# Kernel optimization log

Hardware: AMD Instinct MI355X
Metric: run time of the kernel (lower is better)

The kernel has to match this reference:

```python
import jax, jax.numpy as jnp
import numpy as np

LX, LY = 16, 16
N = 2 * LX * LY        # 512 lattice sites (sequence length)
NH = 128               # GRU hidden size
K = 2                  # binary occupation categories
NS = 4096              # number of Monte-Carlo samples (batch)


def setup_inputs() -> dict:
    key = jax.random.key(0)
    k0, k1, k2, k3 = jax.random.split(key, 4)
    gru_kernel = jax.random.normal(k0, (K, 3 * NH), jnp.float32) * (1.0 / np.sqrt(K))
    gru_rkernel = jax.random.normal(k1, (NH, 3 * NH), jnp.float32) * (1.0 / np.sqrt(NH))
    gru_bias = jnp.zeros((2, 3 * NH), jnp.float32)  # [input_bias; recurrent_bias] (reset_after=True)
    dense_w = jax.random.normal(k2, (NH, K), jnp.float32) * (1.0 / np.sqrt(NH))
    dense_b = jnp.zeros((K,), jnp.float32)
    u = jax.random.uniform(k3, (NS, N), jnp.float32)  # pre-drawn noise for categorical draws
    return {"gru_kernel": gru_kernel, "gru_rkernel": gru_rkernel, "gru_bias": gru_bias,
            "dense_w": dense_w, "dense_b": dense_b, "u": u}


def reference(gru_kernel, gru_rkernel, gru_bias, dense_w, dense_b, u):
    """Autoregressive GRU sampling over N lattice sites.
    Returns (samples [ns,N] int32, log_prob [ns] float32)."""
    ns = u.shape[0]
    b_in, b_rec = gru_bias[0], gru_bias[1]

    def step(carry, u_t):
        h, x = carry                       # h: [ns,NH], x: one-hot prev sample [ns,K]
        xg = x @ gru_kernel + b_in          # [ns,3NH]
        hg = h @ gru_rkernel + b_rec        # [ns,3NH]
        xz, xr, xh = jnp.split(xg, 3, axis=-1)   # keras gate order: z, r, h
        hz, hr, hh = jnp.split(hg, 3, axis=-1)
        z = jax.nn.sigmoid(xz + hz)
        r = jax.nn.sigmoid(xr + hr)
        hc = jnp.tanh(xh + r * hh)          # reset_after=True candidate
        h_new = z * h + (1.0 - z) * hc
        probs = jax.nn.softmax(h_new @ dense_w + dense_b, axis=-1)  # [ns,K]
        p1 = probs[:, 1]
        s = (u_t < p1).astype(jnp.int32)    # categorical draw (K=2) via inverse CDF
        logp_t = jnp.log(jnp.where(s == 1, p1, probs[:, 0]) + 1e-10)
        x_new = jax.nn.one_hot(s, K, dtype=h.dtype)
        return (h_new, x_new), (s, logp_t)

    h0 = jnp.zeros((ns, NH), u.dtype)
    x0 = jnp.zeros((ns, K), u.dtype)        # zero input at first site
    (_, _), (samples, logps) = jax.lax.scan(step, (h0, x0), u.T)  # scan over N sites
    return samples.T, logps.sum(axis=0)
```

## Files before the change

### kernel.cpp

```cpp
#include <hip/hip_runtime.h>

#define NHID   128
#define NSTEPS 512
#define NSAMP  4096
#define SPB    16
#define BS     512
#define NBLK   (NSAMP / SPB)
#define KL4    17
#define SAMP_ELEMS (NSAMP * NSTEPS)
#define WT_ELEMS   (3 * NHID * NHID)

typedef float v2f __attribute__((ext_vector_type(2)));
typedef float v4f __attribute__((ext_vector_type(4)));

#define PK_LO(ACC, W2, H2) \
    asm("v_pk_fma_f32 %0, %1, %2, %0 op_sel:[0,0,0] op_sel_hi:[0,1,1]" \
        : "+v"(ACC) : "v"(W2), "v"(H2))
#define PK_HI(ACC, W2, H2) \
    asm("v_pk_fma_f32 %0, %1, %2, %0 op_sel:[1,0,0] op_sel_hi:[1,1,1]" \
        : "+v"(ACC) : "v"(W2), "v"(H2))

template<int IMM>
__device__ __forceinline__ float swz(float x) {
    return __int_as_float(__builtin_amdgcn_ds_swizzle(__float_as_int(x), IMM));
}

__global__ __launch_bounds__(256)
void pack_w_kernel(const float* __restrict__ rk, float* __restrict__ wt) {
    const int i = blockIdx.x * 256 + threadIdx.x;
    if (i < WT_ELEMS) {
        const int j  = i & 3;
        const int c  = (i >> 2) & 127;
        const int k4 = (i >> 9) & 31;
        const int g  = i >> 14;
        wt[i] = rk[(k4 * 4 + j) * 384 + g * NHID + c];
    }
}

template<int TR>
__global__ __launch_bounds__(BS, 2)
void vmc_gru_kernel(const float* __restrict__ gk,
                    const float* __restrict__ rk,
                    const float* __restrict__ gb,
                    const float* __restrict__ dw,
                    const float* __restrict__ db,
                    const float* __restrict__ u,
                    const float* __restrict__ wt,
                    float* __restrict__ out)
{
    __shared__ float hsm[2][NHID][SPB];
    __shared__ float part[2][8][SPB][2];
    __shared__ float uld[NSTEPS][SPB];
    __shared__ v4f   slds[3 * KL4 * NHID];

    const int tid = threadIdx.x;
    const int cg  = tid >> 2;
    const int sq  = tid & 3;
    const int s0  = sq * 4;
    const int wv  = tid >> 6;

    {
        const int sl = tid >> 5;
        const int t0 = (tid & 31) * 16;
        const float* up = u + (size_t)(blockIdx.x * SPB + sl) * NSTEPS + t0;
        const float4 a = ((const float4*)up)[0];
        const float4 b = ((const float4*)up)[1];
        const float4 c = ((const float4*)up)[2];
        const float4 d = ((const float4*)up)[3];
        const float tmp[16] = {a.x,a.y,a.z,a.w, b.x,b.y,b.z,b.w,
                               c.x,c.y,c.z,c.w, d.x,d.y,d.z,d.w};
        #pragma unroll
        for (int i = 0; i < 16; ++i) uld[t0 + i][sl] = tmp[i];
    }
    if (TR) {
        const v4f* wt4 = (const v4f*)wt;
        for (int i = tid; i < 3 * KL4 * NHID; i += BS) {
            const int g = i / (KL4 * NHID);
            const int r = i - g * (KL4 * NHID);
            slds[i] = wt4[g * 4096 + r];
        }
    }
    for (int i = tid; i < NHID * SPB; i += BS) (&hsm[0][0][0])[i] = 0.0f;
    __syncthreads();

    const float brz = gb[384 + cg];
    const float brr = gb[384 + 128 + cg];
    const float brh = gb[384 + 256 + cg];
    const float xzI = gb[cg],       xz0c = xzI + gk[cg],       xz1c = xzI + gk[384 + cg];
    const float xrI = gb[128 + cg], xr0c = xrI + gk[128 + cg], xr1c = xrI + gk[384 + 128 + cg];
    const float xhI = gb[256 + cg], xh0c = xhI + gk[256 + cg], xh1c = xhI + gk[384 + 256 + cg];
    const float dwc0 = dw[cg * 2], dwc1 = dw[cg * 2 + 1];
    const float db0 = db[0], db1 = db[1];

    const v4f* lz = slds + cg;
    const v4f* lr = slds + KL4 * 128 + cg;
    const v4f* lh = slds + 2 * KL4 * 128 + cg;
    const v4f* wz4 = (const v4f*)wt + cg;
    const v4f* wr4 = (const v4f*)wt + 4096 + cg;
    const v4f* wh4 = (const v4f*)wt + 8192 + cg;
    const float* rkp = rk + cg;

    int   pv[4] = {0, 0, 0, 0};
    float lg[4] = {0.f, 0.f, 0.f, 0.f};
    float pr[4] = {1.f, 1.f, 1.f, 1.f};
    int cur = 0;

    for (int t = 0; t < NSTEPS; ++t) {
        v2f az01 = {brz, brz}, az23 = {brz, brz};
        v2f ar01 = {brr, brr}, ar23 = {brr, brr};
        v2f ah01 = {brh, brh}, ah23 = {brh, brh};
        const float* hb = &hsm[cur][0][0];

#define GEMM_K4(WZ, WR, WH, K4) do {                                      \
    const v4f h0 = *(const v4f*)(hb + (4*(K4)+0)*SPB + s0);               \
    const v4f h1 = *(const v4f*)(hb + (4*(K4)+1)*SPB + s0);               \
    const v4f h2 = *(const v4f*)(hb + (4*(K4)+2)*SPB + s0);               \
    const v4f h3 = *(const v4f*)(hb + (4*(K4)+3)*SPB + s0);               \
    const v2f wzA = (WZ).xy, wzB = (WZ).zw;                               \
    const v2f wrA = (WR).xy, wrB = (WR).zw;                               \
    const v2f whA = (WH).xy, whB = (WH).zw;                               \
    PK_LO(az01, wzA, h0.xy); PK_LO(az23, wzA, h0.zw);                     \
    PK_LO(ar01, wrA, h0.xy); PK_LO(ar23, wrA, h0.zw);                     \
    PK_LO(ah01, whA, h0.xy); PK_LO(ah23, whA, h0.zw);                     \
    PK_HI(az01, wzA, h1.xy); PK_HI(az23, wzA, h1.zw);                     \
    PK_HI(ar01, wrA, h1.xy); PK_HI(ar23, wrA, h1.zw);                     \
    PK_HI(ah01, whA, h1.xy); PK_HI(ah23, whA, h1.zw);                     \
    PK_LO(az01, wzB, h2.xy); PK_LO(az23, wzB, h2.zw);                     \
    PK_LO(ar01, wrB, h2.xy); PK_LO(ar23, wrB, h2.zw);                     \
    PK_LO(ah01, whB, h2.xy); PK_LO(ah23, whB, h2.zw);                     \
    PK_HI(az01, wzB, h3.xy); PK_HI(az23, wzB, h3.zw);                     \
    PK_HI(ar01, wrB, h3.xy); PK_HI(ar23, wrB, h3.zw);                     \
    PK_HI(ah01, whB, h3.xy); PK_HI(ah23, whB, h3.zw);                     \
} while (0)

        if (TR) {
            #pragma unroll 4
            for (int k4 = 0; k4 < KL4; ++k4) {
                const v4f wz = lz[k4 * 128];
                const v4f wr = lr[k4 * 128];
                const v4f wh = lh[k4 * 128];
                GEMM_K4(wz, wr, wh, k4);
            }
            #pragma unroll
            for (int k4 = KL4; k4 < 32; ++k4) {
                const v4f wz = wz4[k4 * 128];
                const v4f wr = wr4[k4 * 128];
                const v4f wh = wh4[k4 * 128];
                GEMM_K4(wz, wr, wh, k4);
            }
        } else {
            const float* wp = rkp;
            #pragma unroll 4
            for (int k = 0; k < NHID; ++k) {
                const float wzs = wp[0];
                const float wrs = wp[NHID];
                const float whs = wp[2 * NHID];
                const v4f hv = *(const v4f*)(hb + k * SPB + s0);
                const float hk[4] = {hv.x, hv.y, hv.z, hv.w};
                float azs[4] = {az01.x, az01.y, az23.x, az23.y};
                float ars[4] = {ar01.x, ar01.y, ar23.x, ar23.y};
                float ahs[4] = {ah01.x, ah01.y, ah23.x, ah23.y};
                #pragma unroll
                for (int j = 0; j < 4; ++j) azs[j] = fmaf(wzs, hk[j], azs[j]);
                #pragma unroll
                for (int j = 0; j < 4; ++j) ars[j] = fmaf(wrs, hk[j], ars[j]);
                #pragma unroll
                for (int j = 0; j < 4; ++j) ahs[j] = fmaf(whs, hk[j], ahs[j]);
                az01 = (v2f){azs[0], azs[1]}; az23 = (v2f){azs[2], azs[3]};
                ar01 = (v2f){ars[0], ars[1]}; ar23 = (v2f){ars[2], ars[3]};
                ah01 = (v2f){ahs[0], ahs[1]}; ah23 = (v2f){ahs[2], ahs[3]};
                wp += 3 * NHID;
            }
        }
#undef GEMM_K4

        const float az[4] = {az01.x, az01.y, az23.x, az23.y};
        const float ar[4] = {ar01.x, ar01.y, ar23.x, ar23.y};
        const float ah[4] = {ah01.x, ah01.y, ah23.x, ah23.y};

        const v4f ho = *(const v4f*)(hb + cg * SPB + s0);
        const float hov[4] = {ho.x, ho.y, ho.z, ho.w};
        float hn[4], p0s[4], p1s[4];
        #pragma unroll
        for (int j = 0; j < 4; ++j) {
            float xz = pv[j] ? xz1c : xz0c;
            float xr = pv[j] ? xr1c : xr0c;
            float xh = pv[j] ? xh1c : xh0c;
            if (t == 0) { xz = xzI; xr = xrI; xh = xhI; }
            const float z  = 1.0f / (1.0f + expf(-(xz + az[j])));
            const float r  = 1.0f / (1.0f + expf(-(xr + ar[j])));
            const float hc = tanhf(xh + r * ah[j]);
            const float hnew = z * hov[j] + (1.0f - z) * hc;
            hn[j] = hnew;
            p0s[j] = hnew * dwc0;
            p1s[j] = hnew * dwc1;
        }
        *(v4f*)&hsm[cur ^ 1][cg][s0] = (v4f){hn[0], hn[1], hn[2], hn[3]};

        #pragma unroll
        for (int j = 0; j < 4; ++j) {
            p0s[j] += swz<0x101F>(p0s[j]);  p1s[j] += swz<0x101F>(p1s[j]);
            p0s[j] += swz<0x201F>(p0s[j]);  p1s[j] += swz<0x201F>(p1s[j]);
            p0s[j] += swz<0x401F>(p0s[j]);  p1s[j] += swz<0x401F>(p1s[j]);
            p0s[j] += __shfl_xor(p0s[j], 32);
            p1s[j] += __shfl_xor(p1s[j], 32);
        }
        const int pb = t & 1;
        if ((tid & 63) < 4) {
            *(float4*)&part[pb][wv][s0][0]     = make_float4(p0s[0], p1s[0], p0s[1], p1s[1]);
            *(float4*)&part[pb][wv][s0 + 2][0] = make_float4(p0s[2], p1s[2], p0s[3], p1s[3]);
        }
        __syncthreads();

        float l0[4] = {db0, db0, db0, db0};
        float l1[4] = {db1, db1, db1, db1};
        #pragma unroll
        for (int w = 0; w < 8; ++w) {
            const float4 qa = *(const float4*)&part[pb][w][s0][0];
            const float4 qb = *(const float4*)&part[pb][w][s0 + 2][0];
            l0[0] += qa.x; l1[0] += qa.y;
            l0[1] += qa.z; l1[1] += qa.w;
            l0[2] += qb.x; l1[2] += qb.y;
            l0[3] += qb.z; l1[3] += qb.w;
        }
        const float4 uu = *(const float4*)&uld[t][s0];
        const float uv[4] = {uu.x, uu.y, uu.z, uu.w};
        #pragma unroll
        for (int j = 0; j < 4; ++j) {
            const float mx = fmaxf(l0[j], l1[j]);
            const float e0 = expf(l0[j] - mx);
            const float e1 = expf(l1[j] - mx);
            const float inv = 1.0f / (e0 + e1);
            const float p1v = e1 * inv;
            const int st = (uv[j] < p1v) ? 1 : 0;
            const float psel = st ? p1v : (e0 * inv);
            pr[j] *= (psel + 1e-10f);
            pv[j] = st;
            if (cg == 0)
                out[(size_t)(blockIdx.x * SPB + s0 + j) * NSTEPS + t] = (float)st;
        }
        if ((t & 7) == 7) {
            #pragma unroll
            for (int j = 0; j < 4; ++j) { lg[j] += logf(pr[j]); pr[j] = 1.0f; }
        }
        cur ^= 1;
    }

    if (cg == 0) {
        #pragma unroll
        for (int j = 0; j < 4; ++j)
            out[SAMP_ELEMS + blockIdx.x * SPB + s0 + j] = lg[j];
    }
}

extern "C" void kernel_launch(void* const* d_in, const int* in_sizes, int n_in,
                              void* d_out, int out_size, void* d_ws, size_t ws_size,
                              hipStream_t stream) {
    const float* gk = (const float*)d_in[0];
    const float* rk = (const float*)d_in[1];
    const float* gb = (const float*)d_in[2];
    const float* dw = (const float*)d_in[3];
    const float* db = (const float*)d_in[4];
    const float* u  = (const float*)d_in[5];
    float* out = (float*)d_out;

    if (ws_size >= (size_t)WT_ELEMS * sizeof(float)) {
        float* wt = (float*)d_ws;
        pack_w_kernel<<<(WT_ELEMS + 255) / 256, 256, 0, stream>>>(rk, wt);
        vmc_gru_kernel<1><<<NBLK, BS, 0, stream>>>(gk, rk, gb, dw, db, u, wt, out);
    } else {
        vmc_gru_kernel<0><<<NBLK, BS, 0, stream>>>(gk, rk, gb, dw, db, u, rk, out);
    }
}
```

Measured before the change: 3.743 ms.

## Map waves to sample quads and broadcast hidden state via readlane to SGPRs

Reorganizes thread mapping so each wave pair owns 4 samples and each lane owns one hidden unit. Hidden state is read once per step into registers and broadcast with readlane into scalar operands of packed FMAs, replacing per-k LDS reads of h. The u staging buffer is removed to make room for more LDS-resident weights (KL 17->20), with u read from global each step, and the partial-sum reduction is reworked accordingly. The scalar readlanes add SALU/VALU dependency latency and the per-step global u loads are uncoalesced.

New measurement: 5.368 ms. 1.43x slower.

```diff
diff --git a/kernel.cpp b/kernel.cpp
--- a/kernel.cpp
+++ b/kernel.cpp
@@ -6,23 +6,45 @@
 #define SPB    16
 #define BS     512
 #define NBLK   (NSAMP / SPB)
-#define KL4    17
+#define KL     20
 #define SAMP_ELEMS (NSAMP * NSTEPS)
 #define WT_ELEMS   (3 * NHID * NHID)
 
 typedef float v2f __attribute__((ext_vector_type(2)));
 typedef float v4f __attribute__((ext_vector_type(4)));
 
-#define PK_LO(ACC, W2, H2) \
+#define PKL(A, W, H) \
     asm("v_pk_fma_f32 %0, %1, %2, %0 op_sel:[0,0,0] op_sel_hi:[0,1,1]" \
-        : "+v"(ACC) : "v"(W2), "v"(H2))
-#define PK_HI(ACC, W2, H2) \
+        : "+v"(A) : "v"(W), "s"(H))
+#define PKH(A, W, H) \
     asm("v_pk_fma_f32 %0, %1, %2, %0 op_sel:[1,0,0] op_sel_hi:[1,1,1]" \
-        : "+v"(ACC) : "v"(W2), "v"(H2))
+        : "+v"(A) : "v"(W), "s"(H))
 
 template<int IMM>
 __device__ __forceinline__ float swz(float x) {
     return __int_as_float(__builtin_amdgcn_ds_swizzle(__float_as_int(x), IMM));
+}
+
+template<int HI>
+__device__ __forceinline__ void pkstep(v4f h, int l, v2f wz, v2f wr, v2f wh,
+                                       v2f& az01, v2f& az23, v2f& ar01,
+                                       v2f& ar23, v2f& ah01, v2f& ah23)
+{
+    const unsigned h0 = (unsigned)__builtin_amdgcn_readlane(__float_as_int(h.x), l);
+    const unsigned h1 = (unsigned)__builtin_amdgcn_readlane(__float_as_int(h.y), l);
+    const unsigned h2 = (unsigned)__builtin_amdgcn_readlane(__float_as_int(h.z), l);
+    const unsigned h3 = (unsigned)__builtin_amdgcn_readlane(__float_as_int(h.w), l);
+    const unsigned long long hp01 = (unsigned long long)h0 | ((unsigned long long)h1 << 32);
+    const unsigned long long hp23 = (unsigned long long)h2 | ((unsigned long long)h3 << 32);
+    if (HI) {
+        PKH(az01, wz, hp01); PKH(az23, wz, hp23);
+        PKH(ar01, wr, hp01); PKH(ar23, wr, hp23);
+        PKH(ah01, wh, hp01); PKH(ah23, wh, hp23);
+    } else {
+        PKL(az01, wz, hp01); PKL(az23, wz, hp23);
+        PKL(ar01, wr, hp01); PKL(ar23, wr, hp23);
+        PKL(ah01, wh, hp01); PKL(ah23, wh, hp23);
+    }
 }
 
 __global__ __launch_bounds__(256)
@@ -48,57 +70,45 @@
                     const float* __restrict__ wt,
                     float* __restrict__ out)
 {
-    __shared__ float hsm[2][NHID][SPB];
-    __shared__ float part[2][8][SPB][2];
-    __shared__ float uld[NSTEPS][SPB];
-    __shared__ v4f   slds[3 * KL4 * NHID];
-
-    const int tid = threadIdx.x;
-    const int cg  = tid >> 2;
-    const int sq  = tid & 3;
-    const int s0  = sq * 4;
-    const int wv  = tid >> 6;
-
-    {
-        const int sl = tid >> 5;
-        const int t0 = (tid & 31) * 16;
-        const float* up = u + (size_t)(blockIdx.x * SPB + sl) * NSTEPS + t0;
-        const float4 a = ((const float4*)up)[0];
-        const float4 b = ((const float4*)up)[1];
-        const float4 c = ((const float4*)up)[2];
-        const float4 d = ((const float4*)up)[3];
-        const float tmp[16] = {a.x,a.y,a.z,a.w, b.x,b.y,b.z,b.w,
-                               c.x,c.y,c.z,c.w, d.x,d.y,d.z,d.w};
-        #pragma unroll
-        for (int i = 0; i < 16; ++i) uld[t0 + i][sl] = tmp[i];
-    }
+    __shared__ v4f   slds[3 * KL * NHID];
+    __shared__ float hsm[2][4][NHID][4];
+    __shared__ float part[2][8][4][8];
+
+    const int tid  = threadIdx.x;
+    const int lane = tid & 63;
+    const int wv   = tid >> 6;
+    const int half = wv & 1;
+    const int q    = wv >> 1;
+    const int c    = half * 64 + lane;
+    const int sbase = blockIdx.x * SPB + q * 4;
+
     if (TR) {
         const v4f* wt4 = (const v4f*)wt;
-        for (int i = tid; i < 3 * KL4 * NHID; i += BS) {
-            const int g = i / (KL4 * NHID);
-            const int r = i - g * (KL4 * NHID);
+        for (int i = tid; i < 3 * KL * NHID; i += BS) {
+            const int g = i / (KL * NHID);
+            const int r = i - g * (KL * NHID);
             slds[i] = wt4[g * 4096 + r];
         }
     }
-    for (int i = tid; i < NHID * SPB; i += BS) (&hsm[0][0][0])[i] = 0.0f;
+    for (int i = tid; i < 2 * 4 * NHID * 4; i += BS) (&hsm[0][0][0][0])[i] = 0.0f;
     __syncthreads();
 
-    const float brz = gb[384 + cg];
-    const float brr = gb[384 + 128 + cg];
-    const float brh = gb[384 + 256 + cg];
-    const float xzI = gb[cg],       xz0c = xzI + gk[cg],       xz1c = xzI + gk[384 + cg];
-    const float xrI = gb[128 + cg], xr0c = xrI + gk[128 + cg], xr1c = xrI + gk[384 + 128 + cg];
-    const float xhI = gb[256 + cg], xh0c = xhI + gk[256 + cg], xh1c = xhI + gk[384 + 256 + cg];
-    const float dwc0 = dw[cg * 2], dwc1 = dw[cg * 2 + 1];
+    const float brz = gb[384 + c];
+    const float brr = gb[384 + 128 + c];
+    const float brh = gb[384 + 256 + c];
+    const float xzI = gb[c],       xz0c = xzI + gk[c],       xz1c = xzI + gk[384 + c];
+    const float xrI = gb[128 + c], xr0c = xrI + gk[128 + c], xr1c = xrI + gk[384 + 128 + c];
+    const float xhI = gb[256 + c], xh0c = xhI + gk[256 + c], xh1c = xhI + gk[384 + 256 + c];
+    const float dwc0 = dw[c * 2], dwc1 = dw[c * 2 + 1];
     const float db0 = db[0], db1 = db[1];
 
-    const v4f* lz = slds + cg;
-    const v4f* lr = slds + KL4 * 128 + cg;
-    const v4f* lh = slds + 2 * KL4 * 128 + cg;
-    const v4f* wz4 = (const v4f*)wt + cg;
-    const v4f* wr4 = (const v4f*)wt + 4096 + cg;
-    const v4f* wh4 = (const v4f*)wt + 8192 + cg;
-    const float* rkp = rk + cg;
+    const v4f* lz = slds + c;
+    const v4f* lr = slds + KL * 128 + c;
+    const v4f* lh = slds + 2 * KL * 128 + c;
+    const v4f* wz4 = (const v4f*)wt + c;
+    const v4f* wr4 = (const v4f*)wt + 4096 + c;
+    const v4f* wh4 = (const v4f*)wt + 8192 + c;
+    const float* rkc = rk + c;
 
     int   pv[4] = {0, 0, 0, 0};
     float lg[4] = {0.f, 0.f, 0.f, 0.f};
@@ -106,79 +116,85 @@
     int cur = 0;
 
     for (int t = 0; t < NSTEPS; ++t) {
+        float uv[4];
+        #pragma unroll
+        for (int j = 0; j < 4; ++j)
+            uv[j] = u[(size_t)(sbase + j) * NSTEPS + t];
+
+        const v4f hA = *(const v4f*)&hsm[cur][q][lane][0];
+        const v4f hB = *(const v4f*)&hsm[cur][q][64 + lane][0];
+
         v2f az01 = {brz, brz}, az23 = {brz, brz};
         v2f ar01 = {brr, brr}, ar23 = {brr, brr};
         v2f ah01 = {brh, brh}, ah23 = {brh, brh};
-        const float* hb = &hsm[cur][0][0];
-
-#define GEMM_K4(WZ, WR, WH, K4) do {                                      \
-    const v4f h0 = *(const v4f*)(hb + (4*(K4)+0)*SPB + s0);               \
-    const v4f h1 = *(const v4f*)(hb + (4*(K4)+1)*SPB + s0);               \
-    const v4f h2 = *(const v4f*)(hb + (4*(K4)+2)*SPB + s0);               \
-    const v4f h3 = *(const v4f*)(hb + (4*(K4)+3)*SPB + s0);               \
-    const v2f wzA = (WZ).xy, wzB = (WZ).zw;                               \
-    const v2f wrA = (WR).xy, wrB = (WR).zw;                               \
-    const v2f whA = (WH).xy, whB = (WH).zw;                               \
-    PK_LO(az01, wzA, h0.xy); PK_LO(az23, wzA, h0.zw);                     \
-    PK_LO(ar01, wrA, h0.xy); PK_LO(ar23, wrA, h0.zw);                     \
-    PK_LO(ah01, whA, h0.xy); PK_LO(ah23, whA, h0.zw);                     \
-    PK_HI(az01, wzA, h1.xy); PK_HI(az23, wzA, h1.zw);                     \
-    PK_HI(ar01, wrA, h1.xy); PK_HI(ar23, wrA, h1.zw);                     \
-    PK_HI(ah01, whA, h1.xy); PK_HI(ah23, whA, h1.zw);                     \
-    PK_LO(az01, wzB, h2.xy); PK_LO(az23, wzB, h2.zw);                     \
-    PK_LO(ar01, wrB, h2.xy); PK_LO(ar23, wrB, h2.zw);                     \
-    PK_LO(ah01, whB, h2.xy); PK_LO(ah23, whB, h2.zw);                     \
-    PK_HI(az01, wzB, h3.xy); PK_HI(az23, wzB, h3.zw);                     \
-    PK_HI(ar01, wrB, h3.xy); PK_HI(ar23, wrB, h3.zw);                     \
-    PK_HI(ah01, whB, h3.xy); PK_HI(ah23, whB, h3.zw);                     \
-} while (0)
 
         if (TR) {
             #pragma unroll 4
-            for (int k4 = 0; k4 < KL4; ++k4) {
-                const v4f wz = lz[k4 * 128];
-                const v4f wr = lr[k4 * 128];
-                const v4f wh = lh[k4 * 128];
-                GEMM_K4(wz, wr, wh, k4);
-            }
-            #pragma unroll
-            for (int k4 = KL4; k4 < 32; ++k4) {
-                const v4f wz = wz4[k4 * 128];
-                const v4f wr = wr4[k4 * 128];
-                const v4f wh = wh4[k4 * 128];
-                GEMM_K4(wz, wr, wh, k4);
+            for (int k4 = 0; k4 < 16; ++k4) {
+                const v4f wzq = lz[k4 * 128];
+                const v4f wrq = lr[k4 * 128];
+                const v4f whq = lh[k4 * 128];
+                const int kb = k4 * 4;
+                pkstep<0>(hA, kb + 0, wzq.xy, wrq.xy, whq.xy, az01, az23, ar01, ar23, ah01, ah23);
+                pkstep<1>(hA, kb + 1, wzq.xy, wrq.xy, whq.xy, az01, az23, ar01, ar23, ah01, ah23);
+                pkstep<0>(hA, kb + 2, wzq.zw, wrq.zw, whq.zw, az01, az23, ar01, ar23, ah01, ah23);
+                pkstep<1>(hA, kb + 3, wzq.zw, wrq.zw, whq.zw, az01, az23, ar01, ar23, ah01, ah23);
+            }
+            #pragma unroll 4
+            for (int k4 = 16; k4 < KL; ++k4) {
+                const v4f wzq = lz[k4 * 128];
+                const v4f wrq = lr[k4 * 128];
+                const v4f whq = lh[k4 * 128];
+                const int kb = k4 * 4 - 64;
+                pkstep<0>(hB, kb + 0, wzq.xy, wrq.xy, whq.xy, az01, az23, ar01, ar23, ah01, ah23);
+                pkstep<1>(hB, kb + 1, wzq.xy, wrq.xy, whq.xy, az01, az23, ar01, ar23, ah01, ah23);
+                pkstep<0>(hB, kb + 2, wzq.zw, wrq.zw, whq.zw, az01, az23, ar01, ar23, ah01, ah23);
+                pkstep<1>(hB, kb + 3, wzq.zw, wrq.zw, whq.zw, az01, az23, ar01, ar23, ah01, ah23);
+            }
+            #pragma unroll 4
+            for (int k4 = KL; k4 < 32; ++k4) {
+                const v4f wzq = wz4[k4 * 128];
+                const v4f wrq = wr4[k4 * 128];
+                const v4f whq = wh4[k4 * 128];
+                const int kb = k4 * 4 - 64;
+                pkstep<0>(hB, kb + 0, wzq.xy, wrq.xy, whq.xy, az01, az23, ar01, ar23, ah01, ah23);
+                pkstep<1>(hB, kb + 1, wzq.xy, wrq.xy, whq.xy, az01, az23, ar01, ar23, ah01, ah23);
+                pkstep<0>(hB, kb + 2, wzq.zw, wrq.zw, whq.zw, az01, az23, ar01, ar23, ah01, ah23);
+                pkstep<1>(hB, kb + 3, wzq.zw, wrq.zw, whq.zw, az01, az23, ar01, ar23, ah01, ah23);
             }
         } else {
-            const float* wp = rkp;
             #pragma unroll 4
             for (int k = 0; k < NHID; ++k) {
-                const float wzs = wp[0];
-                const float wrs = wp[NHID];
-                const float whs = wp[2 * NHID];
-                const v4f hv = *(const v4f*)(hb + k * SPB + s0);
-                const float hk[4] = {hv.x, hv.y, hv.z, hv.w};
+                const v4f hsrc = (k < 64) ? hA : hB;
+                const int l = k & 63;
+                float hh[4];
+                hh[0] = __int_as_float(__builtin_amdgcn_readlane(__float_as_int(hsrc.x), l));
+                hh[1] = __int_as_float(__builtin_amdgcn_readlane(__float_as_int(hsrc.y), l));
+                hh[2] = __int_as_float(__builtin_amdgcn_readlane(__float_as_int(hsrc.z), l));
+                hh[3] = __int_as_float(__builtin_amdgcn_readlane(__float_as_int(hsrc.w), l));
+                const float wzs = rkc[k * 384];
+                const float wrs = rkc[k * 384 + 128];
+                const float whs = rkc[k * 384 + 256];
                 float azs[4] = {az01.x, az01.y, az23.x, az23.y};
                 float ars[4] = {ar01.x, ar01.y, ar23.x, ar23.y};
                 float ahs[4] = {ah01.x, ah01.y, ah23.x, ah23.y};
                 #pragma unroll
-                for (int j = 0; j < 4; ++j) azs[j] = fmaf(wzs, hk[j], azs[j]);
+                for (int j = 0; j < 4; ++j) azs[j] = fmaf(wzs, hh[j], azs[j]);
                 #pragma unroll
-                for (int j = 0; j < 4; ++j) ars[j] = fmaf(wrs, hk[j], ars[j]);
+                for (int j = 0; j < 4; ++j) ars[j] = fmaf(wrs, hh[j], ars[j]);
                 #pragma unroll
-                for (int j = 0; j < 4; ++j) ahs[j] = fmaf(whs, hk[j], ahs[j]);
+                for (int j = 0; j < 4; ++j) ahs[j] = fmaf(whs, hh[j], ahs[j]);
                 az01 = (v2f){azs[0], azs[1]}; az23 = (v2f){azs[2], azs[3]};
                 ar01 = (v2f){ars[0], ars[1]}; ar23 = (v2f){ars[2], ars[3]};
                 ah01 = (v2f){ahs[0], ahs[1]}; ah23 = (v2f){ahs[2], ahs[3]};
-                wp += 3 * NHID;
-            }
-        }
-#undef GEMM_K4
+            }
+        }
 
         const float az[4] = {az01.x, az01.y, az23.x, az23.y};
         const float ar[4] = {ar01.x, ar01.y, ar23.x, ar23.y};
         const float ah[4] = {ah01.x, ah01.y, ah23.x, ah23.y};
 
-        const v4f ho = *(const v4f*)(hb + cg * SPB + s0);
+        const v4f ho = half ? hB : hA;
         const float hov[4] = {ho.x, ho.y, ho.z, ho.w};
         float hn[4], p0s[4], p1s[4];
         #pragma unroll
@@ -195,20 +211,20 @@
             p0s[j] = hnew * dwc0;
             p1s[j] = hnew * dwc1;
         }
-        *(v4f*)&hsm[cur ^ 1][cg][s0] = (v4f){hn[0], hn[1], hn[2], hn[3]};
+        *(v4f*)&hsm[cur ^ 1][q][c][0] = (v4f){hn[0], hn[1], hn[2], hn[3]};
 
         #pragma unroll
         for (int j = 0; j < 4; ++j) {
+            p0s[j] += swz<0x041F>(p0s[j]);  p1s[j] += swz<0x041F>(p1s[j]);
+            p0s[j] += swz<0x081F>(p0s[j]);  p1s[j] += swz<0x081F>(p1s[j]);
             p0s[j] += swz<0x101F>(p0s[j]);  p1s[j] += swz<0x101F>(p1s[j]);
             p0s[j] += swz<0x201F>(p0s[j]);  p1s[j] += swz<0x201F>(p1s[j]);
-            p0s[j] += swz<0x401F>(p0s[j]);  p1s[j] += swz<0x401F>(p1s[j]);
-            p0s[j] += __shfl_xor(p0s[j], 32);
-            p1s[j] += __shfl_xor(p1s[j], 32);
         }
         const int pb = t & 1;
-        if ((tid & 63) < 4) {
-            *(float4*)&part[pb][wv][s0][0]     = make_float4(p0s[0], p1s[0], p0s[1], p1s[1]);
-            *(float4*)&part[pb][wv][s0 + 2][0] = make_float4(p0s[2], p1s[2], p0s[3], p1s[3]);
+        if ((lane & 15) == 0) {
+            const int g = lane >> 4;
+            *(float4*)&part[pb][wv][g][0] = make_float4(p0s[0], p0s[1], p0s[2], p0s[3]);
+            *(float4*)&part[pb][wv][g][4] = make_float4(p1s[0], p1s[1], p1s[2], p1s[3]);
         }
         __syncthreads();
 
@@ -216,15 +232,13 @@
         float l1[4] = {db1, db1, db1, db1};
         #pragma unroll
         for (int w = 0; w < 8; ++w) {
-            const float4 qa = *(const float4*)&part[pb][w][s0][0];
-            const float4 qb = *(const float4*)&part[pb][w][s0 + 2][0];
-            l0[0] += qa.x; l1[0] += qa.y;
-            l0[1] += qa.z; l1[1] += qa.w;
-            l0[2] += qb.x; l1[2] += qb.y;
-            l0[3] += qb.z; l1[3] += qb.w;
-        }
-        const float4 uu = *(const float4*)&uld[t][s0];
-        const float uv[4] = {uu.x, uu.y, uu.z, uu.w};
+            const int hw = w >> 2, g = w & 3;
+            const float4 a = *(const float4*)&part[pb][q * 2 + hw][g][0];
+            const float4 b = *(const float4*)&part[pb][q * 2 + hw][g][4];
+            l0[0] += a.x; l0[1] += a.y; l0[2] += a.z; l0[3] += a.w;
+            l1[0] += b.x; l1[1] += b.y; l1[2] += b.z; l1[3] += b.w;
+        }
+
         #pragma unroll
         for (int j = 0; j < 4; ++j) {
             const float mx = fmaxf(l0[j], l1[j]);
@@ -236,8 +250,8 @@
             const float psel = st ? p1v : (e0 * inv);
             pr[j] *= (psel + 1e-10f);
             pv[j] = st;
-            if (cg == 0)
-                out[(size_t)(blockIdx.x * SPB + s0 + j) * NSTEPS + t] = (float)st;
+            if (lane == 0 && half == 0)
+                out[(size_t)(sbase + j) * NSTEPS + t] = (float)st;
         }
         if ((t & 7) == 7) {
             #pragma unroll
@@ -246,10 +260,10 @@
         cur ^= 1;
     }
 
-    if (cg == 0) {
+    if (lane == 0 && half == 0) {
         #pragma unroll
         for (int j = 0; j < 4; ++j)
-            out[SAMP_ELEMS + blockIdx.x * SPB + s0 + j] = lg[j];
+            out[SAMP_ELEMS + sbase + j] = lg[j];
     }
 }
 
```

## Halve samples per block to double block count and shrink LDS weight slice

Applied to the files above, without the earlier changes.

Blocks now handle 8 samples with 256 threads (2 sample-quads per hidden column) instead of 16 samples with 512 threads, giving 512 blocks instead of 256. The LDS-resident slice of the recurrent weights shrinks from 17 to 11 k-groups, and the uniform noise is read straight from global memory every step instead of being staged in LDS. The partial-logit reduction gains an extra swizzle stage and uses a new part layout. The aim is more independent blocks per CU to hide the serial per-step latency, at the cost of more global weight and noise traffic per sample.

Result: slower. 4.040 ms (+7.9%).

```diff
diff --git a/kernel.cpp b/kernel.cpp
--- a/kernel.cpp
+++ b/kernel.cpp
@@ -3,10 +3,10 @@
 #define NHID   128
 #define NSTEPS 512
 #define NSAMP  4096
-#define SPB    16
-#define BS     512
+#define SPB    8
+#define BS     256
 #define NBLK   (NSAMP / SPB)
-#define KL4    17
+#define KL4    11
 #define SAMP_ELEMS (NSAMP * NSTEPS)
 #define WT_ELEMS   (3 * NHID * NHID)
 
@@ -49,29 +49,16 @@
                     float* __restrict__ out)
 {
     __shared__ float hsm[2][NHID][SPB];
-    __shared__ float part[2][8][SPB][2];
-    __shared__ float uld[NSTEPS][SPB];
+    __shared__ float part[2][4][2][8];
     __shared__ v4f   slds[3 * KL4 * NHID];
 
     const int tid = threadIdx.x;
-    const int cg  = tid >> 2;
-    const int sq  = tid & 3;
+    const int cg  = tid >> 1;
+    const int sq  = tid & 1;
     const int s0  = sq * 4;
     const int wv  = tid >> 6;
-
-    {
-        const int sl = tid >> 5;
-        const int t0 = (tid & 31) * 16;
-        const float* up = u + (size_t)(blockIdx.x * SPB + sl) * NSTEPS + t0;
-        const float4 a = ((const float4*)up)[0];
-        const float4 b = ((const float4*)up)[1];
-        const float4 c = ((const float4*)up)[2];
-        const float4 d = ((const float4*)up)[3];
-        const float tmp[16] = {a.x,a.y,a.z,a.w, b.x,b.y,b.z,b.w,
-                               c.x,c.y,c.z,c.w, d.x,d.y,d.z,d.w};
-        #pragma unroll
-        for (int i = 0; i < 16; ++i) uld[t0 + i][sl] = tmp[i];
-    }
+    const int sbase = blockIdx.x * SPB + s0;
+
     if (TR) {
         const v4f* wt4 = (const v4f*)wt;
         for (int i = tid; i < 3 * KL4 * NHID; i += BS) {
@@ -80,7 +67,7 @@
             slds[i] = wt4[g * 4096 + r];
         }
     }
-    for (int i = tid; i < NHID * SPB; i += BS) (&hsm[0][0][0])[i] = 0.0f;
+    for (int i = tid; i < 2 * NHID * SPB; i += BS) (&hsm[0][0][0])[i] = 0.0f;
     __syncthreads();
 
     const float brz = gb[384 + cg];
@@ -106,6 +93,11 @@
     int cur = 0;
 
     for (int t = 0; t < NSTEPS; ++t) {
+        float uv[4];
+        #pragma unroll
+        for (int j = 0; j < 4; ++j)
+            uv[j] = u[(size_t)(sbase + j) * NSTEPS + t];
+
         v2f az01 = {brz, brz}, az23 = {brz, brz};
         v2f ar01 = {brr, brr}, ar23 = {brr, brr};
         v2f ah01 = {brh, brh}, ah23 = {brh, brh};
@@ -141,7 +133,7 @@
                 const v4f wh = lh[k4 * 128];
                 GEMM_K4(wz, wr, wh, k4);
             }
-            #pragma unroll
+            #pragma unroll 4
             for (int k4 = KL4; k4 < 32; ++k4) {
                 const v4f wz = wz4[k4 * 128];
                 const v4f wr = wr4[k4 * 128];
@@ -199,6 +191,7 @@
 
         #pragma unroll
         for (int j = 0; j < 4; ++j) {
+            p0s[j] += swz<0x081F>(p0s[j]);  p1s[j] += swz<0x081F>(p1s[j]);
             p0s[j] += swz<0x101F>(p0s[j]);  p1s[j] += swz<0x101F>(p1s[j]);
             p0s[j] += swz<0x201F>(p0s[j]);  p1s[j] += swz<0x201F>(p1s[j]);
             p0s[j] += swz<0x401F>(p0s[j]);  p1s[j] += swz<0x401F>(p1s[j]);
@@ -206,25 +199,21 @@
             p1s[j] += __shfl_xor(p1s[j], 32);
         }
         const int pb = t & 1;
-        if ((tid & 63) < 4) {
-            *(float4*)&part[pb][wv][s0][0]     = make_float4(p0s[0], p1s[0], p0s[1], p1s[1]);
-            *(float4*)&part[pb][wv][s0 + 2][0] = make_float4(p0s[2], p1s[2], p0s[3], p1s[3]);
+        if ((tid & 63) < 2) {
+            *(float4*)&part[pb][wv][sq][0] = make_float4(p0s[0], p0s[1], p0s[2], p0s[3]);
+            *(float4*)&part[pb][wv][sq][4] = make_float4(p1s[0], p1s[1], p1s[2], p1s[3]);
         }
         __syncthreads();
 
         float l0[4] = {db0, db0, db0, db0};
         float l1[4] = {db1, db1, db1, db1};
         #pragma unroll
-        for (int w = 0; w < 8; ++w) {
-            const float4 qa = *(const float4*)&part[pb][w][s0][0];
-            const float4 qb = *(const float4*)&part[pb][w][s0 + 2][0];
-            l0[0] += qa.x; l1[0] += qa.y;
-            l0[1] += qa.z; l1[1] += qa.w;
-            l0[2] += qb.x; l1[2] += qb.y;
-            l0[3] += qb.z; l1[3] += qb.w;
-        }
-        const float4 uu = *(const float4*)&uld[t][s0];
-        const float uv[4] = {uu.x, uu.y, uu.z, uu.w};
+        for (int w = 0; w < 4; ++w) {
+            const float4 a = *(const float4*)&part[pb][w][sq][0];
+            const float4 b = *(const float4*)&part[pb][w][sq][4];
+            l0[0] += a.x; l0[1] += a.y; l0[2] += a.z; l0[3] += a.w;
+            l1[0] += b.x; l1[1] += b.y; l1[2] += b.z; l1[3] += b.w;
+        }
         #pragma unroll
         for (int j = 0; j < 4; ++j) {
             const float mx = fmaxf(l0[j], l1[j]);
@@ -237,7 +226,7 @@
             pr[j] *= (psel + 1e-10f);
             pv[j] = st;
             if (cg == 0)
-                out[(size_t)(blockIdx.x * SPB + s0 + j) * NSTEPS + t] = (float)st;
+                out[(size_t)(sbase + j) * NSTEPS + t] = (float)st;
         }
         if ((t & 7) == 7) {
             #pragma unroll
@@ -249,7 +238,7 @@
     if (cg == 0) {
         #pragma unroll
         for (int j = 0; j < 4; ++j)
-            out[SAMP_ELEMS + blockIdx.x * SPB + s0 + j] = lg[j];
+            out[SAMP_ELEMS + sbase + j] = lg[j];
     }
 }
 
```
